# Performance work log

Hardware: AMD Instinct MI355X
Metric: run time of the kernel (lower is better)

Reference implementation:

```python
import jax, jax.numpy as jnp
import numpy as np

H, D = 20, 64  # heads, head_dim (hidden_size = 1280)


def setup_inputs() -> dict:
    key = jax.random.key(0)
    ks = jax.random.split(key, 10)
    B, S, HID, CROSS, T_TXT, T_IP = 8, 4096, 1280, 2048, 77, 4
    w = lambda k, shp: jax.random.normal(k, shp, dtype=jnp.float32) * 0.02
    return {
        "hidden_states": jax.random.normal(ks[0], (B, S, HID), dtype=jnp.float32),
        "encoder_hidden_states": jax.random.normal(ks[1], (B, T_TXT, CROSS), dtype=jnp.float32),
        "ip_hidden_states": jax.random.normal(ks[2], (B, T_IP, CROSS), dtype=jnp.float32),
        "Wq": w(ks[3], (HID, HID)),
        "Wk": w(ks[4], (CROSS, HID)),
        "Wv": w(ks[5], (CROSS, HID)),
        "Wk_ip": w(ks[6], (CROSS, HID)),
        "Wv_ip": w(ks[7], (CROSS, HID)),
        "Wo": w(ks[8], (HID, HID)),
        "bo": jnp.zeros((HID,), dtype=jnp.float32),
    }


def _attend(q, kv_in, Wk, Wv):
    # q: [B,S,H,D]; kv_in: [B,T,cross]
    B, T = kv_in.shape[0], kv_in.shape[1]
    k = (kv_in @ Wk).reshape(B, T, H, D)
    v = (kv_in @ Wv).reshape(B, T, H, D)
    scale = 1.0 / jnp.sqrt(jnp.asarray(D, q.dtype))
    scores = jnp.einsum("bqhd,bkhd->bhqk", q, k) * scale
    probs = jax.nn.softmax(scores, axis=-1)
    out = jnp.einsum("bhqk,bkhd->bqhd", probs, v)
    return out.reshape(B, q.shape[1], H * D)


def reference(hidden_states, encoder_hidden_states, ip_hidden_states,
              Wq, Wk, Wv, Wk_ip, Wv_ip, Wo, bo):
    B, S, _ = hidden_states.shape
    q = (hidden_states @ Wq).reshape(B, S, H, D)
    # text cross-attention branch
    out = _attend(q, encoder_hidden_states, Wk, Wv)
    # IP-adapter branch (single adapter, scale=1.0, no mask)
    ip_scale = 1.0
    out = out + ip_scale * _attend(q, ip_hidden_states, Wk_ip, Wv_ip)
    # output projection (dropout is identity at inference)
    return out @ Wo + bo
```

## Files before the change

kernel.cpp:

```cpp
#include <hip/hip_runtime.h>

using u16 = unsigned short;
using u32 = unsigned int;
typedef __bf16 bf16x8 __attribute__((ext_vector_type(8)));
typedef float f32x4 __attribute__((ext_vector_type(4)));
typedef float f32x16 __attribute__((ext_vector_type(16)));

__device__ __forceinline__ u16 f2bf(float f) {
  u32 u = __float_as_uint(f);
  u += 0x7FFFu + ((u >> 16) & 1u);
  return (u16)(u >> 16);
}

__device__ __forceinline__ u32 cvtpk(float a, float b) {
  u32 r;
  asm("v_cvt_pk_bf16_f32 %0, %1, %2" : "=v"(r) : "v"(a), "v"(b));
  return r;
}

__device__ __forceinline__ void gload16(const u16* g, u16* l) {
  __builtin_amdgcn_global_load_lds((const __attribute__((address_space(1))) void*)g,
                                   (__attribute__((address_space(3))) void*)l, 16, 0, 0);
}

__global__ void prep_all(const float* __restrict__ enc, const float* __restrict__ ip,
                         u16* __restrict__ a_all,
                         const float* __restrict__ Wk, const float* __restrict__ Wv,
                         const float* __restrict__ Wkip, const float* __restrict__ Wvip,
                         u16* __restrict__ kvw,
                         const float* __restrict__ Wq, const float* __restrict__ Wo,
                         u16* __restrict__ wq_t, u16* __restrict__ wo_t) {
  const int bid = blockIdx.x;
  const int tid = threadIdx.x;
  if (bid < 1536) {
    const int i = bid * 256 + tid;
    const int row = i >> 9;
    const int c4 = i & 511;
    ushort4 o = {0, 0, 0, 0};
    const float4* src = nullptr;
    if (row < 616) src = (const float4*)enc + (size_t)row * 512 + c4;
    else if (row >= 640 && row < 672) src = (const float4*)ip + (size_t)(row - 640) * 512 + c4;
    if (src) {
      const float4 v = *src;
      o.x = f2bf(v.x); o.y = f2bf(v.y); o.z = f2bf(v.z); o.w = f2bf(v.w);
    }
    ((ushort4*)a_all)[i] = o;
    return;
  }
  __shared__ float tile[32][33];
  const int x = tid & 31, y = tid >> 5;
  const float* in;
  u16* out;
  int K, N, n0, k0;
  if (bid < 11776) {
    const int f = bid - 1536;
    const int z = f / 2560, rem = f % 2560;
    in = (z == 0) ? Wk : (z == 1) ? Wv : (z == 2) ? Wkip : Wvip;
    out = kvw + (size_t)z * 1280 * 2048;
    K = 2048; N = 1280;
    n0 = (rem % 40) << 5; k0 = (rem / 40) << 5;
  } else {
    const int f = bid - 11776;
    const int z = f / 1600, rem = f % 1600;
    in = z ? Wo : Wq;
    out = z ? wo_t : wq_t;
    K = 1280; N = 1280;
    n0 = (rem % 40) << 5; k0 = (rem / 40) << 5;
  }
#pragma unroll
  for (int i = 0; i < 32; i += 8)
    tile[y + i][x] = in[(size_t)(k0 + y + i) * N + n0 + x];
  __syncthreads();
#pragma unroll
  for (int i = 0; i < 32; i += 8)
    out[(size_t)(n0 + y + i) * K + k0 + x] = f2bf(tile[x][y + i]);
}

#define MFMA16(a, b, c) __builtin_amdgcn_mfma_f32_16x16x32_bf16(a, b, c, 0, 0, 0)
#define MFMA32(a, b, c) __builtin_amdgcn_mfma_f32_32x32x16_bf16(a, b, c, 0, 0, 0)

template <int MODE, int CONV>
__global__ __launch_bounds__(512, 2) void gemm256(
    const u16* __restrict__ A, const u16* __restrict__ Bt,
    u16* __restrict__ Cb, const u16* __restrict__ ktP, const u16* __restrict__ vtP,
    const float* __restrict__ convSrc, u16* __restrict__ convDst,
    int M, int N, int K) {
  const int tid = threadIdx.x;

  if (CONV) {
    if (blockIdx.x >= 60) {
      const float4* src = (const float4*)convSrc;
      ushort4* dst = (ushort4*)convDst;
      const long base = (long)(blockIdx.x - 60) * 4096 + tid;
#pragma unroll
      for (int k = 0; k < 8; ++k) {
        const float4 v = src[base + k * 512];
        ushort4 o;
        o.x = f2bf(v.x); o.y = f2bf(v.y); o.z = f2bf(v.z); o.w = f2bf(v.w);
        dst[base + k * 512] = o;
      }
      return;
    }
  }

  __shared__ __align__(16) u16 smem[67584];
  u16* As = smem;
  u16* Bs = smem + 32768;

  const int w = tid >> 6, lane = tid & 63;
  const int lo = lane & 15, hi = lane >> 4;
  const int wm = w >> 2, wn = w & 3;

  const int nbn = N >> 8;
  int wg = blockIdx.x;
  if (!CONV) {
    const int nwg = gridDim.x;
    const int q = nwg >> 3, r = nwg & 7;
    const int xcd = wg & 7, l = wg >> 3;
    wg = (xcd < r ? xcd * (q + 1) : r * (q + 1) + (xcd - r) * q) + l;
  }
  const int bm = wg / nbn, bn = wg % nbn;
  const int m0 = bm << 8, n0 = bn << 8;
  const int NT = K >> 6;

  const int sr = lane >> 3;
  const int sc8 = ((lane & 7) ^ sr) << 3;
  const u16* pA[2];
  const u16* pB[2];
#pragma unroll
  for (int i = 0; i < 2; ++i) {
    const int rr = (i * 8 + w) * 8 + sr;
    pA[i] = A + (size_t)(m0 + rr) * K + sc8;
    pB[i] = Bt + (size_t)(n0 + rr) * K + sc8;
  }
  const int ch0 = w * 512, ch1 = (8 + w) * 512;

#define STAGE_A(h, tt)                                                     \
  {                                                                        \
    const int ttc = ((tt) < NT) ? (tt) : (NT - 1);                         \
    u16* d = As + ((((tt)&1) * 2 + (h)) << 13);                            \
    const size_t off = (size_t)(h)*128 * K + (size_t)ttc * 64;             \
    gload16(pA[0] + off, d + ch0);                                         \
    gload16(pA[1] + off, d + ch1);                                         \
  }
#define STAGE_B(h, tt)                                                     \
  {                                                                        \
    const int ttc = ((tt) < NT) ? (tt) : (NT - 1);                         \
    u16* d = Bs + ((((tt)&1) * 2 + (h)) << 13);                            \
    const size_t off = (size_t)(h)*128 * K + (size_t)ttc * 64;             \
    gload16(pB[0] + off, d + ch0);                                         \
    gload16(pB[1] + off, d + ch1);                                         \
  }

  const int low0 = (lo << 7) | ((hi ^ (lo & 7)) << 4);
  const int low1 = (lo << 7) | (((4 | hi) ^ (lo & 7)) << 4);

  f32x4 acc[8][4];
#pragma unroll
  for (int i = 0; i < 8; ++i)
#pragma unroll
    for (int j = 0; j < 4; ++j) acc[i][j] = (f32x4){0.f, 0.f, 0.f, 0.f};

  STAGE_B(0, 0); STAGE_B(1, 0);
  STAGE_A(0, 0); STAGE_A(1, 0);
  STAGE_B(0, 1); STAGE_B(1, 1);

  const char* aSm = (const char*)As;
  const char* bSm = (const char*)Bs;

  for (int t = 0; t < NT; ++t) {
    const int p = t & 1;
    const int aBase = (p * 2 + wm) << 14;
    const int bBase = ((p * 2 + (wn >> 1)) << 14) + ((wn & 1) << 13);

    asm volatile("s_waitcnt vmcnt(4)" ::: "memory");
    asm volatile("s_barrier" ::: "memory");

    bf16x8 a0[4][2], a1[4][2], b0[2][2], b1[2][2];
#pragma unroll
    for (int mf = 0; mf < 4; ++mf) {
      a0[mf][0] = *(const bf16x8*)(aSm + aBase + (mf << 11) + low0);
      a0[mf][1] = *(const bf16x8*)(aSm + aBase + (mf << 11) + low1);
    }
#pragma unroll
    for (int nf = 0; nf < 2; ++nf) {
      b0[nf][0] = *(const bf16x8*)(bSm + bBase + (nf << 11) + low0);
      b0[nf][1] = *(const bf16x8*)(bSm + bBase + (nf << 11) + low1);
    }
    STAGE_A(0, t + 1);
    __builtin_amdgcn_s_setprio(1);
#pragma unroll
    for (int mf = 0; mf < 4; ++mf)
#pragma unroll
      for (int nf = 0; nf < 2; ++nf) {
        acc[mf][nf] = MFMA16(a0[mf][0], b0[nf][0], acc[mf][nf]);
        acc[mf][nf] = MFMA16(a0[mf][1], b0[nf][1], acc[mf][nf]);
      }
    __builtin_amdgcn_s_setprio(0);

#pragma unroll
    for (int nf = 0; nf < 2; ++nf) {
      b1[nf][0] = *(const bf16x8*)(bSm + bBase + (1 << 12) + (nf << 11) + low0);
      b1[nf][1] = *(const bf16x8*)(bSm + bBase + (1 << 12) + (nf << 11) + low1);
    }
    STAGE_A(1, t + 1);
    __builtin_amdgcn_s_setprio(1);
#pragma unroll
    for (int mf = 0; mf < 4; ++mf)
#pragma unroll
      for (int nf = 0; nf < 2; ++nf) {
        acc[mf][2 + nf] = MFMA16(a0[mf][0], b1[nf][0], acc[mf][2 + nf]);
        acc[mf][2 + nf] = MFMA16(a0[mf][1], b1[nf][1], acc[mf][2 + nf]);
      }
    __builtin_amdgcn_s_setprio(0);
    asm volatile("s_barrier" ::: "memory");

#pragma unroll
    for (int mf = 0; mf < 4; ++mf) {
      a1[mf][0] = *(const bf16x8*)(aSm + aBase + (1 << 13) + (mf << 11) + low0);
      a1[mf][1] = *(const bf16x8*)(aSm + aBase + (1 << 13) + (mf << 11) + low1);
    }
    STAGE_B(0, t + 2);
    __builtin_amdgcn_s_setprio(1);
#pragma unroll
    for (int mf = 0; mf < 4; ++mf)
#pragma unroll
      for (int nf = 0; nf < 2; ++nf) {
        acc[4 + mf][nf] = MFMA16(a1[mf][0], b0[nf][0], acc[4 + mf][nf]);
        acc[4 + mf][nf] = MFMA16(a1[mf][1], b0[nf][1], acc[4 + mf][nf]);
      }
    __builtin_amdgcn_s_setprio(0);

    STAGE_B(1, t + 2);
    __builtin_amdgcn_s_setprio(1);
#pragma unroll
    for (int mf = 0; mf < 4; ++mf)
#pragma unroll
      for (int nf = 0; nf < 2; ++nf) {
        acc[4 + mf][2 + nf] = MFMA16(a1[mf][0], b1[nf][0], acc[4 + mf][2 + nf]);
        acc[4 + mf][2 + nf] = MFMA16(a1[mf][1], b1[nf][1], acc[4 + mf][2 + nf]);
      }
    __builtin_amdgcn_s_setprio(0);
  }

  if (MODE != 2) {
#pragma unroll
    for (int g = 0; g < 2; ++g)
#pragma unroll
      for (int mf = 0; mf < 4; ++mf)
#pragma unroll
        for (int ng = 0; ng < 2; ++ng)
#pragma unroll
          for (int nfi = 0; nfi < 2; ++nfi) {
            const f32x4 v = acc[g * 4 + mf][ng * 2 + nfi];
            const int row0 = m0 + wm * 128 + g * 64 + mf * 16 + hi * 4;
            const int col = n0 + wn * 64 + ng * 32 + nfi * 16 + lo;
#pragma unroll
            for (int r = 0; r < 4; ++r)
              Cb[(size_t)(row0 + r) * N + col] = f2bf(v[r]);
          }
  } else {
    const int l31 = lane & 31, hi5 = lane >> 5;
    const int h = bn * 4 + wn;
    const int b = m0 >> 12;
    const u16* ktb = ktP + (size_t)(b * 20 + h) * 6144;
    const u16* vtb = vtP + (size_t)(b * 20 + h) * 6144;

    bf16x8 kreg[3][4];
#pragma unroll
    for (int kf = 0; kf < 3; ++kf)
#pragma unroll
      for (int dc = 0; dc < 4; ++dc)
        kreg[kf][dc] = *(const bf16x8*)(ktb + (((kf << 2) | dc) << 9) + lane * 8);

    asm volatile("s_waitcnt vmcnt(0)" ::: "memory");
    __builtin_amdgcn_s_barrier();

    u16* qlds = smem + w * 8448;
#pragma unroll
    for (int g = 0; g < 2; ++g)
#pragma unroll
      for (int mf = 0; mf < 4; ++mf)
#pragma unroll
        for (int ng = 0; ng < 2; ++ng)
#pragma unroll
          for (int nfi = 0; nfi < 2; ++nfi) {
            const f32x4 v = acc[g * 4 + mf][ng * 2 + nfi];
            const int qrow = g * 64 + mf * 16 + hi * 4;
            const int d = ng * 32 + nfi * 16 + lo;
#pragma unroll
            for (int r = 0; r < 4; ++r) qlds[(qrow + r) * 66 + d] = f2bf(v[r]);
          }

    const int rowB = m0 + wm * 128;

#pragma unroll
    for (int pass = 0; pass < 2; ++pass) {
      bf16x8 qf0[4], qf1[4];
#pragma unroll
      for (int dc = 0; dc < 4; ++dc) {
        qf0[dc] = *(const bf16x8*)&qlds[(pass * 64 + l31) * 66 + dc * 16 + hi5 * 8];
        qf1[dc] = *(const bf16x8*)&qlds[(pass * 64 + 32 + l31) * 66 + dc * 16 + hi5 * 8];
      }

      f32x16 s0[3], s1[3];
#pragma unroll
      for (int kf = 0; kf < 3; ++kf)
#pragma unroll
        for (int r = 0; r < 16; ++r) { s0[kf][r] = 0.f; s1[kf][r] = 0.f; }

#pragma unroll
      for (int kf = 0; kf < 3; ++kf)
#pragma unroll
        for (int dc = 0; dc < 4; ++dc) {
          s0[kf] = MFMA32(kreg[kf][dc], qf0[dc], s0[kf]);
          s1[kf] = MFMA32(kreg[kf][dc], qf1[dc], s1[kf]);
        }

      float st0 = 0.f, si0 = 0.f, st1 = 0.f, si1 = 0.f;
#pragma unroll
      for (int kf = 0; kf < 3; ++kf)
#pragma unroll
        for (int r = 0; r < 16; ++r) {
          const int krem = (r & 3) + 8 * (r >> 2);
          const int k = kf * 32 + krem + 4 * hi5;
          const bool vtx = k < 77;
          const bool vip = (k >= 80) & (k < 84);
          const float e0 = (vtx | vip) ? __expf(s0[kf][r] * 0.125f) : 0.f;
          const float e1 = (vtx | vip) ? __expf(s1[kf][r] * 0.125f) : 0.f;
          s0[kf][r] = e0; s1[kf][r] = e1;
          st0 += vtx ? e0 : 0.f; si0 += vip ? e0 : 0.f;
          st1 += vtx ? e1 : 0.f; si1 += vip ? e1 : 0.f;
        }
      st0 += __shfl_xor(st0, 32); si0 += __shfl_xor(si0, 32);
      st1 += __shfl_xor(st1, 32); si1 += __shfl_xor(si1, 32);
      const float rt0 = __fdividef(1.f, st0), ri0 = __fdividef(1.f, si0);
      const float rt1 = __fdividef(1.f, st1), ri1 = __fdividef(1.f, si1);
#pragma unroll
      for (int kf = 0; kf < 3; ++kf)
#pragma unroll
        for (int r = 0; r < 16; ++r) {
          const int krem = (r & 3) + 8 * (r >> 2);
          const int k = kf * 32 + krem + 4 * hi5;
          const bool vip = (k >= 80) & (k < 84);
          s0[kf][r] *= vip ? ri0 : rt0;
          s1[kf][r] *= vip ? ri1 : rt1;
        }

#define PV_STORE(sA, qoff)                                                  \
      {                                                                     \
        f32x16 pacc[2];                                                     \
        _Pragma("unroll") for (int nf = 0; nf < 2; ++nf)                    \
        _Pragma("unroll") for (int r = 0; r < 16; ++r) pacc[nf][r] = 0.f;   \
        _Pragma("unroll") for (int ks = 0; ks < 6; ++ks) {                  \
          const int kf = ks >> 1;                                           \
          const int rb = (ks & 1) * 8;                                      \
          const u32 lo01 = cvtpk(sA[kf][rb + 0], sA[kf][rb + 1]);           \
          const u32 lo23 = cvtpk(sA[kf][rb + 2], sA[kf][rb + 3]);           \
          const u32 hi01 = cvtpk(sA[kf][rb + 4], sA[kf][rb + 5]);           \
          const u32 hi23 = cvtpk(sA[kf][rb + 6], sA[kf][rb + 7]);           \
          const u32 plo01 = __shfl_xor(lo01, 32);                           \
          const u32 plo23 = __shfl_xor(lo23, 32);                           \
          const u32 phi01 = __shfl_xor(hi01, 32);                           \
          const u32 phi23 = __shfl_xor(hi23, 32);                           \
          union { u32 u[4]; bf16x8 v; } pu;                                 \
          pu.u[0] = hi5 ? phi01 : lo01;                                     \
          pu.u[1] = hi5 ? phi23 : lo23;                                     \
          pu.u[2] = hi5 ? hi01 : plo01;                                     \
          pu.u[3] = hi5 ? hi23 : plo23;                                     \
          _Pragma("unroll") for (int nf = 0; nf < 2; ++nf) {                \
            const bf16x8 vb = *(const bf16x8*)(vtb +                        \
                ((((hi5 * 2 + nf) * 6 + ks) * 32 + l31) << 3));             \
            pacc[nf] = MFMA32(pu.v, vb, pacc[nf]);                          \
          }                                                                 \
        }                                                                   \
        _Pragma("unroll") for (int nf = 0; nf < 2; ++nf)                    \
        _Pragma("unroll") for (int r = 0; r < 16; ++r) {                    \
          const int row = rowB + pass * 64 + (qoff) +                       \
                          (r & 3) + 8 * (r >> 2) + 4 * hi5;                 \
          Cb[(size_t)row * 1280 + h * 64 + nf * 32 + l31] =                 \
              f2bf(pacc[nf][r]);                                            \
        }                                                                   \
      }

      PV_STORE(s0, 0)
      PV_STORE(s1, 32)
#undef PV_STORE
    }
  }
#undef STAGE_A
#undef STAGE_B
}

__global__ __launch_bounds__(256, 2) void gemm128(
    const u16* __restrict__ A, const u16* __restrict__ Bt,
    float* __restrict__ Cf, const float* __restrict__ bias,
    int M, int N, int K) {
  __shared__ __align__(16) u16 smem[32768];
  const int tid = threadIdx.x;
  const int w = tid >> 6, lane = tid & 63;
  const int lo = lane & 15, hi = lane >> 4;
  const int wm = w >> 1, wn = w & 1;

  const int nbn = N >> 7;
  int wg = blockIdx.x;
  {
    const int nwg = gridDim.x;
    const int q = nwg >> 3, r = nwg & 7;
    const int xcd = wg & 7, l = wg >> 3;
    wg = (xcd < r ? xcd * (q + 1) : r * (q + 1) + (xcd - r) * q) + l;
  }
  const int bm = wg / nbn, bn = wg % nbn;
  const int m0 = bm << 7, n0 = bn << 7;
  const int NT = K >> 6;

  const int sr = lane >> 3;
  const int sc8 = ((lane & 7) ^ sr) << 3;
  const u16 *pA[4], *pB[4];
#pragma unroll
  for (int j = 0; j < 4; ++j) {
    const int rr = (w + j * 4) * 8 + sr;
    pA[j] = A + (size_t)(m0 + rr) * K + sc8;
    pB[j] = Bt + (size_t)(n0 + rr) * K + sc8;
  }

#define STG128(tt)                                                         \
  {                                                                        \
    const int ttc = ((tt) < NT) ? (tt) : (NT - 1);                         \
    const int bofs = (((tt)&1) << 13);          \
    const size_t off = (size_t)ttc * 64;                                   \
    _Pragma("unroll") for (int j = 0; j < 4; ++j) {                        \
      gload16(pA[j] + off, smem + bofs + (w + j * 4) * 512);               \
      gload16(pB[j] + off, smem + 16384 + bofs + (w + j * 4) * 512);       \
    }                                                                      \
  }

  const int low0 = (lo << 7) | ((hi ^ (lo & 7)) << 4);
  const int low1 = (lo << 7) | (((4 | hi) ^ (lo & 7)) << 4);
  const char* aSm = (const char*)smem;
  const char* bSm = (const char*)(smem + 16384);

  f32x4 acc[4][4];
#pragma unroll
  for (int i = 0; i < 4; ++i)
#pragma unroll
    for (int j = 0; j < 4; ++j) acc[i][j] = (f32x4){0.f, 0.f, 0.f, 0.f};

  STG128(0); STG128(1);

  for (int t = 0; t < NT; ++t) {
    const int aBase = ((t & 1) << 14) + (wm << 13);
    const int bBase = ((t & 1) << 14) + (wn << 13);

    asm volatile("s_waitcnt vmcnt(8)" ::: "memory");
    asm volatile("s_barrier" ::: "memory");

    bf16x8 a[4][2], b[4][2];
#pragma unroll
    for (int mf = 0; mf < 4; ++mf) {
      a[mf][0] = *(const bf16x8*)(aSm + aBase + (mf << 11) + low0);
      a[mf][1] = *(const bf16x8*)(aSm + aBase + (mf << 11) + low1);
    }
#pragma unroll
    for (int nf = 0; nf < 4; ++nf) {
      b[nf][0] = *(const bf16x8*)(bSm + bBase + (nf << 11) + low0);
      b[nf][1] = *(const bf16x8*)(bSm + bBase + (nf << 11) + low1);
    }
    asm volatile("s_waitcnt lgkmcnt(0)" ::: "memory");
    __builtin_amdgcn_sched_barrier(0);
    asm volatile("s_barrier" ::: "memory");
    STG128(t + 2);
    __builtin_amdgcn_s_setprio(1);
#pragma unroll
    for (int mf = 0; mf < 4; ++mf)
#pragma unroll
      for (int nf = 0; nf < 4; ++nf) {
        acc[mf][nf] = MFMA16(a[mf][0], b[nf][0], acc[mf][nf]);
        acc[mf][nf] = MFMA16(a[mf][1], b[nf][1], acc[mf][nf]);
      }
    __builtin_amdgcn_s_setprio(0);
  }

#pragma unroll
  for (int mf = 0; mf < 4; ++mf)
#pragma unroll
    for (int nf = 0; nf < 4; ++nf) {
      const int row0 = m0 + wm * 64 + mf * 16 + hi * 4;
      const int col = n0 + wn * 64 + nf * 16 + lo;
      const float bb = bias[col];
#pragma unroll
      for (int r = 0; r < 4; ++r)
        Cf[(size_t)(row0 + r) * N + col] = acc[mf][nf][r] + bb;
    }
#undef STG128
}

__global__ __launch_bounds__(256) void build_kvt(const u16* __restrict__ kvc,
                                                 u16* __restrict__ kt2,
                                                 u16* __restrict__ vt2) {
  __shared__ u16 Ls[96][72];
  const int tid = threadIdx.x;
  const int h = blockIdx.x % 20, b = blockIdx.x / 20;

  for (int idx = tid; idx < 96 * 8; idx += 256) {
    const int row = idx >> 3, c8 = (idx & 7) << 3;
    uint4 val = make_uint4(0, 0, 0, 0);
    if (row < 77)
      val = *(const uint4*)(kvc + (size_t)(b * 77 + row) * 5120 + 1280 + h * 64 + c8);
    else if (row >= 80 && row < 84)
      val = *(const uint4*)(kvc + (size_t)(640 + b * 4 + row - 80) * 5120 + 3840 + h * 64 + c8);
    *(uint4*)&Ls[row][c8] = val;
  }

  u16* kdst = kt2 + (size_t)blockIdx.x * 6144;
  for (int idx = tid; idx < 768; idx += 256) {
    const int lane_ = idx & 63;
    const int rest = idx >> 6;
    const int dc = rest & 3, kf = rest >> 2;
    const int key = kf * 32 + (lane_ & 31);
    const int dofs = dc * 16 + (lane_ >> 5) * 8;
    const u16* src;
    if (key < 77) src = kvc + (size_t)(b * 77 + key) * 5120 + h * 64 + dofs;
    else if (key >= 80 && key < 84)
      src = kvc + (size_t)(640 + b * 4 + key - 80) * 5120 + 2560 + h * 64 + dofs;
    else src = kvc + h * 64 + dofs;
    *(uint4*)(kdst + idx * 8) = *(const uint4*)src;
  }
  __syncthreads();

  u16* vdst = vt2 + (size_t)blockIdx.x * 6144;
  for (int idx = tid; idx < 768; idx += 256) {
    const int l31 = idx & 31;
    const int rest = idx >> 5;
    const int ks = rest % 6;
    const int t = rest / 6;
    const int nf = t & 1, hi5 = t >> 1;
    u16 tmp[8];
#pragma unroll
    for (int j = 0; j < 8; ++j) tmp[j] = Ls[ks * 16 + hi5 * 8 + j][nf * 32 + l31];
    *(uint4*)(vdst + (((size_t)(hi5 * 2 + nf) * 6 + ks) * 32 + l31) * 8) = *(const uint4*)tmp;
  }
}

extern "C" void kernel_launch(void* const* d_in, const int* in_sizes, int n_in,
                              void* d_out, int out_size, void* d_ws, size_t ws_size,
                              hipStream_t stream) {
  (void)in_sizes; (void)n_in; (void)out_size; (void)ws_size;
  const float* hs   = (const float*)d_in[0];
  const float* enc  = (const float*)d_in[1];
  const float* ip   = (const float*)d_in[2];
  const float* Wq   = (const float*)d_in[3];
  const float* Wk   = (const float*)d_in[4];
  const float* Wv   = (const float*)d_in[5];
  const float* Wkip = (const float*)d_in[6];
  const float* Wvip = (const float*)d_in[7];
  const float* Wo   = (const float*)d_in[8];
  const float* bo   = (const float*)d_in[9];
  float* out = (float*)d_out;

  u16* wq_t  = (u16*)d_out;
  u16* hs_bf = (u16*)d_out + 41943040;

  char* ws = (char*)d_ws;
  u16* kvc   = (u16*)(ws);
  u16* wo_t  = (u16*)(ws + 15728640);
  u16* kt2   = (u16*)(ws + 19005440);
  u16* vt2   = (u16*)(ws + 20971520);
  u16* attn  = (u16*)(ws + 22937600);
  u16* kvw   = (u16*)(ws + 22937600 + 3276800);
  u16* a_all = (u16*)(ws + 22937600 + 24248320);

  prep_all<<<14976, 256, 0, stream>>>(enc, ip, a_all, Wk, Wv, Wkip, Wvip, kvw,
                                      Wq, Wo, wq_t, wo_t);

  gemm256<0, 1><<<2620, 512, 0, stream>>>(a_all, kvw, kvc, nullptr, nullptr,
                                          hs, hs_bf, 768, 5120, 2048);
  build_kvt<<<160, 256, 0, stream>>>(kvc, kt2, vt2);

  gemm256<2, 0><<<640, 512, 0, stream>>>(hs_bf, wq_t, attn, kt2, vt2,
                                         nullptr, nullptr, 32768, 1280, 1280);

  gemm128<<<2560, 256, 0, stream>>>(attn, wo_t, out, bo, 32768, 1280, 1280);
}
```

Baseline: 328.6 us.

## Move fused Q-projection attention epilogue from 256-tile to 128-tile GEMM

The Q projection with its fused cross-attention epilogue now runs in the 128x128, 256-thread GEMM instead of the 256x256, 512-thread one. Each wave handles one head with 64 query rows, processed as two 32-row groups in a non-unrolled loop. The aim is more workgroups (2560 vs 640) for better load balance across CUs and lower register pressure in the epilogue. The trade-off is less operand reuse in the GEMM mainloop and more redundant K/V register loads per head. The KV GEMM becomes a non-template kernel and drops its XCD remap.

```diff
diff --git a/kernel.cpp b/kernel.cpp
--- a/kernel.cpp
+++ b/kernel.cpp
@@ -79,31 +79,27 @@
 #define MFMA16(a, b, c) __builtin_amdgcn_mfma_f32_16x16x32_bf16(a, b, c, 0, 0, 0)
 #define MFMA32(a, b, c) __builtin_amdgcn_mfma_f32_32x32x16_bf16(a, b, c, 0, 0, 0)
 
-template <int MODE, int CONV>
-__global__ __launch_bounds__(512, 2) void gemm256(
-    const u16* __restrict__ A, const u16* __restrict__ Bt,
-    u16* __restrict__ Cb, const u16* __restrict__ ktP, const u16* __restrict__ vtP,
+__global__ __launch_bounds__(512, 2) void gemm256kv(
+    const u16* __restrict__ A, const u16* __restrict__ Bt, u16* __restrict__ Cb,
     const float* __restrict__ convSrc, u16* __restrict__ convDst,
     int M, int N, int K) {
   const int tid = threadIdx.x;
 
-  if (CONV) {
-    if (blockIdx.x >= 60) {
-      const float4* src = (const float4*)convSrc;
-      ushort4* dst = (ushort4*)convDst;
-      const long base = (long)(blockIdx.x - 60) * 4096 + tid;
-#pragma unroll
-      for (int k = 0; k < 8; ++k) {
-        const float4 v = src[base + k * 512];
-        ushort4 o;
-        o.x = f2bf(v.x); o.y = f2bf(v.y); o.z = f2bf(v.z); o.w = f2bf(v.w);
-        dst[base + k * 512] = o;
-      }
-      return;
-    }
-  }
-
-  __shared__ __align__(16) u16 smem[67584];
+  if (blockIdx.x >= 60) {
+    const float4* src = (const float4*)convSrc;
+    ushort4* dst = (ushort4*)convDst;
+    const long base = (long)(blockIdx.x - 60) * 4096 + tid;
+#pragma unroll
+    for (int k = 0; k < 8; ++k) {
+      const float4 v = src[base + k * 512];
+      ushort4 o;
+      o.x = f2bf(v.x); o.y = f2bf(v.y); o.z = f2bf(v.z); o.w = f2bf(v.w);
+      dst[base + k * 512] = o;
+    }
+    return;
+  }
+
+  __shared__ __align__(16) u16 smem[65536];
   u16* As = smem;
   u16* Bs = smem + 32768;
 
@@ -112,13 +108,7 @@
   const int wm = w >> 2, wn = w & 3;
 
   const int nbn = N >> 8;
-  int wg = blockIdx.x;
-  if (!CONV) {
-    const int nwg = gridDim.x;
-    const int q = nwg >> 3, r = nwg & 7;
-    const int xcd = wg & 7, l = wg >> 3;
-    wg = (xcd < r ? xcd * (q + 1) : r * (q + 1) + (xcd - r) * q) + l;
-  }
+  const int wg = blockIdx.x;
   const int bm = wg / nbn, bn = wg % nbn;
   const int m0 = bm << 8, n0 = bn << 8;
   const int NT = K >> 6;
@@ -243,158 +233,30 @@
     __builtin_amdgcn_s_setprio(0);
   }
 
-  if (MODE != 2) {
-#pragma unroll
-    for (int g = 0; g < 2; ++g)
-#pragma unroll
-      for (int mf = 0; mf < 4; ++mf)
-#pragma unroll
-        for (int ng = 0; ng < 2; ++ng)
-#pragma unroll
-          for (int nfi = 0; nfi < 2; ++nfi) {
-            const f32x4 v = acc[g * 4 + mf][ng * 2 + nfi];
-            const int row0 = m0 + wm * 128 + g * 64 + mf * 16 + hi * 4;
-            const int col = n0 + wn * 64 + ng * 32 + nfi * 16 + lo;
-#pragma unroll
-            for (int r = 0; r < 4; ++r)
-              Cb[(size_t)(row0 + r) * N + col] = f2bf(v[r]);
-          }
-  } else {
-    const int l31 = lane & 31, hi5 = lane >> 5;
-    const int h = bn * 4 + wn;
-    const int b = m0 >> 12;
-    const u16* ktb = ktP + (size_t)(b * 20 + h) * 6144;
-    const u16* vtb = vtP + (size_t)(b * 20 + h) * 6144;
-
-    bf16x8 kreg[3][4];
-#pragma unroll
-    for (int kf = 0; kf < 3; ++kf)
-#pragma unroll
-      for (int dc = 0; dc < 4; ++dc)
-        kreg[kf][dc] = *(const bf16x8*)(ktb + (((kf << 2) | dc) << 9) + lane * 8);
-
-    asm volatile("s_waitcnt vmcnt(0)" ::: "memory");
-    __builtin_amdgcn_s_barrier();
-
-    u16* qlds = smem + w * 8448;
-#pragma unroll
-    for (int g = 0; g < 2; ++g)
-#pragma unroll
-      for (int mf = 0; mf < 4; ++mf)
-#pragma unroll
-        for (int ng = 0; ng < 2; ++ng)
-#pragma unroll
-          for (int nfi = 0; nfi < 2; ++nfi) {
-            const f32x4 v = acc[g * 4 + mf][ng * 2 + nfi];
-            const int qrow = g * 64 + mf * 16 + hi * 4;
-            const int d = ng * 32 + nfi * 16 + lo;
-#pragma unroll
-            for (int r = 0; r < 4; ++r) qlds[(qrow + r) * 66 + d] = f2bf(v[r]);
-          }
-
-    const int rowB = m0 + wm * 128;
-
-#pragma unroll
-    for (int pass = 0; pass < 2; ++pass) {
-      bf16x8 qf0[4], qf1[4];
-#pragma unroll
-      for (int dc = 0; dc < 4; ++dc) {
-        qf0[dc] = *(const bf16x8*)&qlds[(pass * 64 + l31) * 66 + dc * 16 + hi5 * 8];
-        qf1[dc] = *(const bf16x8*)&qlds[(pass * 64 + 32 + l31) * 66 + dc * 16 + hi5 * 8];
-      }
-
-      f32x16 s0[3], s1[3];
-#pragma unroll
-      for (int kf = 0; kf < 3; ++kf)
-#pragma unroll
-        for (int r = 0; r < 16; ++r) { s0[kf][r] = 0.f; s1[kf][r] = 0.f; }
-
-#pragma unroll
-      for (int kf = 0; kf < 3; ++kf)
-#pragma unroll
-        for (int dc = 0; dc < 4; ++dc) {
-          s0[kf] = MFMA32(kreg[kf][dc], qf0[dc], s0[kf]);
-          s1[kf] = MFMA32(kreg[kf][dc], qf1[dc], s1[kf]);
+#pragma unroll
+  for (int g = 0; g < 2; ++g)
+#pragma unroll
+    for (int mf = 0; mf < 4; ++mf)
+#pragma unroll
+      for (int ng = 0; ng < 2; ++ng)
+#pragma unroll
+        for (int nfi = 0; nfi < 2; ++nfi) {
+          const f32x4 v = acc[g * 4 + mf][ng * 2 + nfi];
+          const int row0 = m0 + wm * 128 + g * 64 + mf * 16 + hi * 4;
+          const int col = n0 + wn * 64 + ng * 32 + nfi * 16 + lo;
+#pragma unroll
+          for (int r = 0; r < 4; ++r)
+            Cb[(size_t)(row0 + r) * N + col] = f2bf(v[r]);
         }
-
-      float st0 = 0.f, si0 = 0.f, st1 = 0.f, si1 = 0.f;
-#pragma unroll
-      for (int kf = 0; kf < 3; ++kf)
-#pragma unroll
-        for (int r = 0; r < 16; ++r) {
-          const int krem = (r & 3) + 8 * (r >> 2);
-          const int k = kf * 32 + krem + 4 * hi5;
-          const bool vtx = k < 77;
-          const bool vip = (k >= 80) & (k < 84);
-          const float e0 = (vtx | vip) ? __expf(s0[kf][r] * 0.125f) : 0.f;
-          const float e1 = (vtx | vip) ? __expf(s1[kf][r] * 0.125f) : 0.f;
-          s0[kf][r] = e0; s1[kf][r] = e1;
-          st0 += vtx ? e0 : 0.f; si0 += vip ? e0 : 0.f;
-          st1 += vtx ? e1 : 0.f; si1 += vip ? e1 : 0.f;
-        }
-      st0 += __shfl_xor(st0, 32); si0 += __shfl_xor(si0, 32);
-      st1 += __shfl_xor(st1, 32); si1 += __shfl_xor(si1, 32);
-      const float rt0 = __fdividef(1.f, st0), ri0 = __fdividef(1.f, si0);
-      const float rt1 = __fdividef(1.f, st1), ri1 = __fdividef(1.f, si1);
-#pragma unroll
-      for (int kf = 0; kf < 3; ++kf)
-#pragma unroll
-        for (int r = 0; r < 16; ++r) {
-          const int krem = (r & 3) + 8 * (r >> 2);
-          const int k = kf * 32 + krem + 4 * hi5;
-          const bool vip = (k >= 80) & (k < 84);
-          s0[kf][r] *= vip ? ri0 : rt0;
-          s1[kf][r] *= vip ? ri1 : rt1;
-        }
-
-#define PV_STORE(sA, qoff)                                                  \
-      {                                                                     \
-        f32x16 pacc[2];                                                     \
-        _Pragma("unroll") for (int nf = 0; nf < 2; ++nf)                    \
-        _Pragma("unroll") for (int r = 0; r < 16; ++r) pacc[nf][r] = 0.f;   \
-        _Pragma("unroll") for (int ks = 0; ks < 6; ++ks) {                  \
-          const int kf = ks >> 1;                                           \
-          const int rb = (ks & 1) * 8;                                      \
-          const u32 lo01 = cvtpk(sA[kf][rb + 0], sA[kf][rb + 1]);           \
-          const u32 lo23 = cvtpk(sA[kf][rb + 2], sA[kf][rb + 3]);           \
-          const u32 hi01 = cvtpk(sA[kf][rb + 4], sA[kf][rb + 5]);           \
-          const u32 hi23 = cvtpk(sA[kf][rb + 6], sA[kf][rb + 7]);           \
-          const u32 plo01 = __shfl_xor(lo01, 32);                           \
-          const u32 plo23 = __shfl_xor(lo23, 32);                           \
-          const u32 phi01 = __shfl_xor(hi01, 32);                           \
-          const u32 phi23 = __shfl_xor(hi23, 32);                           \
-          union { u32 u[4]; bf16x8 v; } pu;                                 \
-          pu.u[0] = hi5 ? phi01 : lo01;                                     \
-          pu.u[1] = hi5 ? phi23 : lo23;                                     \
-          pu.u[2] = hi5 ? hi01 : plo01;                                     \
-          pu.u[3] = hi5 ? hi23 : plo23;                                     \
-          _Pragma("unroll") for (int nf = 0; nf < 2; ++nf) {                \
-            const bf16x8 vb = *(const bf16x8*)(vtb +                        \
-                ((((hi5 * 2 + nf) * 6 + ks) * 32 + l31) << 3));             \
-            pacc[nf] = MFMA32(pu.v, vb, pacc[nf]);                          \
-          }                                                                 \
-        }                                                                   \
-        _Pragma("unroll") for (int nf = 0; nf < 2; ++nf)                    \
-        _Pragma("unroll") for (int r = 0; r < 16; ++r) {                    \
-          const int row = rowB + pass * 64 + (qoff) +                       \
-                          (r & 3) + 8 * (r >> 2) + 4 * hi5;                 \
-          Cb[(size_t)row * 1280 + h * 64 + nf * 32 + l31] =                 \
-              f2bf(pacc[nf][r]);                                            \
-        }                                                                   \
-      }
-
-      PV_STORE(s0, 0)
-      PV_STORE(s1, 32)
-#undef PV_STORE
-    }
-  }
 #undef STAGE_A
 #undef STAGE_B
 }
 
+template <int MODE>
 __global__ __launch_bounds__(256, 2) void gemm128(
     const u16* __restrict__ A, const u16* __restrict__ Bt,
-    float* __restrict__ Cf, const float* __restrict__ bias,
+    u16* __restrict__ Cb, float* __restrict__ Cf, const float* __restrict__ bias,
+    const u16* __restrict__ ktP, const u16* __restrict__ vtP,
     int M, int N, int K) {
   __shared__ __align__(16) u16 smem[32768];
   const int tid = threadIdx.x;
@@ -481,17 +343,135 @@
     __builtin_amdgcn_s_setprio(0);
   }
 
-#pragma unroll
-  for (int mf = 0; mf < 4; ++mf)
-#pragma unroll
-    for (int nf = 0; nf < 4; ++nf) {
-      const int row0 = m0 + wm * 64 + mf * 16 + hi * 4;
-      const int col = n0 + wn * 64 + nf * 16 + lo;
-      const float bb = bias[col];
-#pragma unroll
-      for (int r = 0; r < 4; ++r)
-        Cf[(size_t)(row0 + r) * N + col] = acc[mf][nf][r] + bb;
-    }
+  if (MODE == 1) {
+#pragma unroll
+    for (int mf = 0; mf < 4; ++mf)
+#pragma unroll
+      for (int nf = 0; nf < 4; ++nf) {
+        const int row0 = m0 + wm * 64 + mf * 16 + hi * 4;
+        const int col = n0 + wn * 64 + nf * 16 + lo;
+        const float bb = bias[col];
+#pragma unroll
+        for (int r = 0; r < 4; ++r)
+          Cf[(size_t)(row0 + r) * N + col] = acc[mf][nf][r] + bb;
+      }
+  } else {
+    const int l31 = lane & 31, hi5 = lane >> 5;
+    const int h = bn * 2 + wn;
+    const int b = m0 >> 12;
+    const u16* ktb = ktP + (size_t)(b * 20 + h) * 6144;
+    const u16* vtb = vtP + (size_t)(b * 20 + h) * 6144;
+
+    bf16x8 kreg[3][4];
+#pragma unroll
+    for (int kf = 0; kf < 3; ++kf)
+#pragma unroll
+      for (int dc = 0; dc < 4; ++dc)
+        kreg[kf][dc] = *(const bf16x8*)(ktb + (((kf << 2) | dc) << 9) + lane * 8);
+
+    asm volatile("s_waitcnt vmcnt(0)" ::: "memory");
+    __builtin_amdgcn_s_barrier();
+
+    u16* qlds = smem + w * 4224;
+#pragma unroll
+    for (int mf = 0; mf < 4; ++mf)
+#pragma unroll
+      for (int nf = 0; nf < 4; ++nf) {
+        const f32x4 v = acc[mf][nf];
+        const int qrow = mf * 16 + hi * 4;
+        const int d = nf * 16 + lo;
+#pragma unroll
+        for (int r = 0; r < 4; ++r) qlds[(qrow + r) * 66 + d] = f2bf(v[r]);
+      }
+    asm volatile("s_waitcnt lgkmcnt(0)" ::: "memory");
+    __builtin_amdgcn_sched_barrier(0);
+
+    const int rowB = m0 + wm * 64;
+
+#pragma unroll 1
+    for (int grp = 0; grp < 2; ++grp) {
+      bf16x8 qf[4];
+#pragma unroll
+      for (int dc = 0; dc < 4; ++dc)
+        qf[dc] = *(const bf16x8*)&qlds[(grp * 32 + l31) * 66 + dc * 16 + hi5 * 8];
+
+      f32x16 s[3];
+#pragma unroll
+      for (int kf = 0; kf < 3; ++kf)
+#pragma unroll
+        for (int r = 0; r < 16; ++r) s[kf][r] = 0.f;
+
+#pragma unroll
+      for (int kf = 0; kf < 3; ++kf)
+#pragma unroll
+        for (int dc = 0; dc < 4; ++dc) s[kf] = MFMA32(kreg[kf][dc], qf[dc], s[kf]);
+
+      float st = 0.f, si = 0.f;
+#pragma unroll
+      for (int kf = 0; kf < 3; ++kf)
+#pragma unroll
+        for (int r = 0; r < 16; ++r) {
+          const int krem = (r & 3) + 8 * (r >> 2);
+          const int k = kf * 32 + krem + 4 * hi5;
+          const bool vtx = k < 77;
+          const bool vip = (k >= 80) & (k < 84);
+          const float e = (vtx | vip) ? __expf(s[kf][r] * 0.125f) : 0.f;
+          s[kf][r] = e;
+          st += vtx ? e : 0.f;
+          si += vip ? e : 0.f;
+        }
+      st += __shfl_xor(st, 32);
+      si += __shfl_xor(si, 32);
+      const float rt = __fdividef(1.f, st);
+      const float ri = __fdividef(1.f, si);
+#pragma unroll
+      for (int kf = 0; kf < 3; ++kf)
+#pragma unroll
+        for (int r = 0; r < 16; ++r) {
+          const int krem = (r & 3) + 8 * (r >> 2);
+          const int k = kf * 32 + krem + 4 * hi5;
+          const bool vip = (k >= 80) & (k < 84);
+          s[kf][r] *= vip ? ri : rt;
+        }
+
+      f32x16 pacc[2];
+#pragma unroll
+      for (int nf = 0; nf < 2; ++nf)
+#pragma unroll
+        for (int r = 0; r < 16; ++r) pacc[nf][r] = 0.f;
+#pragma unroll
+      for (int ks = 0; ks < 6; ++ks) {
+        const int kf = ks >> 1;
+        const int rb = (ks & 1) * 8;
+        const u32 lo01 = cvtpk(s[kf][rb + 0], s[kf][rb + 1]);
+        const u32 lo23 = cvtpk(s[kf][rb + 2], s[kf][rb + 3]);
+        const u32 hi01 = cvtpk(s[kf][rb + 4], s[kf][rb + 5]);
+        const u32 hi23 = cvtpk(s[kf][rb + 6], s[kf][rb + 7]);
+        const u32 plo01 = __shfl_xor(lo01, 32);
+        const u32 plo23 = __shfl_xor(lo23, 32);
+        const u32 phi01 = __shfl_xor(hi01, 32);
+        const u32 phi23 = __shfl_xor(hi23, 32);
+        union { u32 u[4]; bf16x8 v; } pu;
+        pu.u[0] = hi5 ? phi01 : lo01;
+        pu.u[1] = hi5 ? phi23 : lo23;
+        pu.u[2] = hi5 ? hi01 : plo01;
+        pu.u[3] = hi5 ? hi23 : plo23;
+#pragma unroll
+        for (int nf = 0; nf < 2; ++nf) {
+          const bf16x8 vb = *(const bf16x8*)(vtb +
+              ((((hi5 * 2 + nf) * 6 + ks) * 32 + l31) << 3));
+          pacc[nf] = MFMA32(pu.v, vb, pacc[nf]);
+        }
+      }
+#pragma unroll
+      for (int nf = 0; nf < 2; ++nf)
+#pragma unroll
+        for (int r = 0; r < 16; ++r) {
+          const int row = rowB + grp * 32 + (r & 3) + 8 * (r >> 2) + 4 * hi5;
+          Cb[(size_t)row * 1280 + h * 64 + nf * 32 + l31] = f2bf(pacc[nf][r]);
+        }
+    }
+  }
 #undef STG128
 }
 
@@ -573,12 +553,12 @@
   prep_all<<<14976, 256, 0, stream>>>(enc, ip, a_all, Wk, Wv, Wkip, Wvip, kvw,
                                       Wq, Wo, wq_t, wo_t);
 
-  gemm256<0, 1><<<2620, 512, 0, stream>>>(a_all, kvw, kvc, nullptr, nullptr,
-                                          hs, hs_bf, 768, 5120, 2048);
+  gemm256kv<<<2620, 512, 0, stream>>>(a_all, kvw, kvc, hs, hs_bf, 768, 5120, 2048);
   build_kvt<<<160, 256, 0, stream>>>(kvc, kt2, vt2);
 
-  gemm256<2, 0><<<640, 512, 0, stream>>>(hs_bf, wq_t, attn, kt2, vt2,
-                                         nullptr, nullptr, 32768, 1280, 1280);
-
-  gemm128<<<2560, 256, 0, stream>>>(attn, wo_t, out, bo, 32768, 1280, 1280);
-}
+  gemm128<2><<<2560, 256, 0, stream>>>(hs_bf, wq_t, attn, nullptr, nullptr,
+                                       kt2, vt2, 32768, 1280, 1280);
+
+  gemm128<1><<<2560, 256, 0, stream>>>(attn, wo_t, nullptr, out, bo,
+                                       nullptr, nullptr, 32768, 1280, 1280);
+}
```

Measured after the change: 341.2 us. 1.04x slower.
